# Optimization experiments

Measured on AMD Instinct MI355X. Metric: run time of the kernel, lower is better.

## Reference

```python
import jax, jax.numpy as jnp
import numpy as np

SIGMA = 1e-4
GAMMA = 1e-4
ZNEAR = 1.0
ZFAR = 100.0
EPS = 1e-10
BG = (1.0, 1.0, 1.0)

N, H, W, K = 4, 512, 512, 8
V, F = 100000, 200000


def setup_inputs() -> dict:
    key = jax.random.key(0)
    k1, k2, k3, k4, k5, k6 = jax.random.split(key, 6)
    pix_to_face = jax.random.randint(k1, (N, H, W, K), -1, F)  # -1 = background
    bary = jax.random.uniform(k2, (N, H, W, K, 3), dtype=jnp.float32)
    bary = bary / jnp.sum(bary, axis=-1, keepdims=True)  # valid barycentric
    zbuf = ZNEAR + (ZFAR - ZNEAR) * jax.random.uniform(k3, (N, H, W, K), dtype=jnp.float32)
    dists = 1e-4 * jax.random.normal(k4, (N, H, W, K), dtype=jnp.float32)
    verts_normals = jax.random.normal(k5, (V, 3), dtype=jnp.float32)
    verts_normals = verts_normals / jnp.linalg.norm(verts_normals, axis=-1, keepdims=True)
    faces = jax.random.randint(k6, (F, 3), 0, V)
    return {"pix_to_face": pix_to_face, "bary_coords": bary, "zbuf": zbuf,
            "dists": dists, "verts_normals": verts_normals, "faces": faces}


def reference(pix_to_face, bary_coords, zbuf, dists, verts_normals, faces):
    # --- NormalCalcuate: gather per-face vertex normals + barycentric interp ---
    faces_normals = verts_normals[faces]                      # (F, 3verts, 3)
    mask = pix_to_face >= 0                                    # (N,H,W,K)
    idx = jnp.maximum(pix_to_face, 0)
    attrs = faces_normals[idx]                                 # (N,H,W,K,3verts,3)
    pixel_normals = jnp.einsum('nhwkv,nhwkvd->nhwkd', bary_coords, attrs)
    pixel_normals = jnp.where(mask[..., None], pixel_normals, 0.0)

    # --- softmax_rgb_blend ---
    m = mask.astype(pixel_normals.dtype)
    prob_map = jax.nn.sigmoid(-dists / SIGMA) * m              # (N,H,W,K)
    z_inv = (ZFAR - zbuf) / (ZFAR - ZNEAR) * m                 # (N,H,W,K)
    z_inv_max = jnp.maximum(jnp.max(z_inv, axis=-1, keepdims=True), EPS)
    weights_num = prob_map * jnp.exp((z_inv - z_inv_max) / GAMMA)
    delta = jnp.maximum(jnp.exp((EPS - z_inv_max[..., 0]) / GAMMA), EPS)  # (N,H,W)
    denom = jnp.sum(weights_num, axis=-1) + delta              # (N,H,W)
    weighted_colors = jnp.einsum('nhwk,nhwkd->nhwd', weights_num, pixel_normals)
    bg = jnp.asarray(BG, dtype=pixel_normals.dtype)
    rgb = (weighted_colors + delta[..., None] * bg) / denom[..., None]  # (N,H,W,3)

    # --- F.normalize(dim=3) then (x+1)/2 ---
    norm = jnp.maximum(jnp.linalg.norm(rgb, axis=-1, keepdims=True), 1e-12)
    images = (rgb / norm + 1.0) / 2.0
    return images
```

## Files before the change

kernel.cpp:

```cpp
#include <hip/hip_runtime.h>

#define SIGMA_INV 1.0e4f
#define GAMMA_INV 1.0e4f
#define ZNEAR 1.0f
#define ZFAR 100.0f
#define EPSV 1e-10f

constexpr int KF = 8;
constexpr int NPIX = 4 * 512 * 512;
constexpr int NFACES = 200000;
#define LOG_CUT (-16.0f)
#define ZWIN (16.0f / GAMMA_INV)
#define ZMAX_SAFE 0.01f

typedef int      i32x4 __attribute__((ext_vector_type(4)));
typedef float    f32x4 __attribute__((ext_vector_type(4)));
typedef unsigned u32x4 __attribute__((ext_vector_type(4)));
typedef float    f32x2 __attribute__((ext_vector_type(2), aligned(4)));

__global__ __launch_bounds__(256) void pack_face_normals14(
    const int*   __restrict__ faces,
    const float* __restrict__ vnorm,
    uint4*       __restrict__ fn,
    int F)
{
    const int f = blockIdx.x * blockDim.x + threadIdx.x;
    if (f >= F) return;
    const int v[3] = { faces[f * 3 + 0], faces[f * 3 + 1], faces[f * 3 + 2] };

    unsigned long long lo = 0ull, hi = 0ull;
    int i = 0;
#pragma unroll
    for (int t = 0; t < 3; ++t) {
#pragma unroll
        for (int c = 0; c < 3; ++c, ++i) {
            const float x = vnorm[(size_t)v[t] * 3 + c];
            const unsigned long long code = (unsigned long long)(unsigned)
                __float2int_rn(fminf(fmaxf(x, -1.0f), 1.0f) * 8191.5f + 8191.5f);
            const int bp = 14 * i;
            if (bp < 64) {
                lo |= code << bp;
                if (bp > 50) hi |= code >> (64 - bp);
            } else {
                hi |= code << (bp - 64);
            }
        }
    }
    uint4 q;
    q.x = (unsigned)(lo & 0xFFFFFFFFull);
    q.y = (unsigned)(lo >> 32);
    q.z = (unsigned)(hi & 0xFFFFFFFFull);
    q.w = (unsigned)(hi >> 32);
    fn[f] = q;
}

__device__ __forceinline__ float dec14(const unsigned* w, int i) {
    const int bp = 14 * i;
    const int j = bp >> 5;
    const int off = bp & 31;
    unsigned long long u = (unsigned long long)w[j];
    if (j < 3) u |= (unsigned long long)w[j + 1] << 32;
    const unsigned code = (unsigned)(u >> off) & 0x3FFFu;
    return fmaf((float)code, 2.0f / 16383.0f, -1.0f);
}

__global__ __launch_bounds__(256) void normal_shader_q14_split(
    const int*   __restrict__ p2f,
    const float* __restrict__ bary,
    const float* __restrict__ zbuf,
    const float* __restrict__ dists,
    const uint4* __restrict__ fn,
    float*       __restrict__ out)
{
    const int p = blockIdx.x * blockDim.x + threadIdx.x;
    if (p >= NPIX) return;

    const int*   pfp = p2f + (size_t)p * KF;
    const float* zp  = zbuf + (size_t)p * KF;

    i32x4 fa, fb;
    f32x4 za, zb;
    asm volatile(
        "global_load_dwordx4 %0, %4, off sc0\n\t"
        "global_load_dwordx4 %1, %5, off sc0\n\t"
        "global_load_dwordx4 %2, %6, off sc0\n\t"
        "global_load_dwordx4 %3, %7, off sc0\n\t"
        "s_waitcnt vmcnt(0)"
        : "=&v"(fa), "=&v"(fb), "=&v"(za), "=&v"(zb)
        : "v"(pfp), "v"(pfp + 4), "v"(zp), "v"(zp + 4)
        : "memory");

    int f[KF] = {fa[0], fa[1], fa[2], fa[3], fb[0], fb[1], fb[2], fb[3]};
    float zv[KF] = {za[0], za[1], za[2], za[3], zb[0], zb[1], zb[2], zb[3]};

    float zinv[KF];
    float zmax = EPSV;
#pragma unroll
    for (int k = 0; k < KF; ++k) {
        const float zi = (f[k] >= 0) ? (ZFAR - zv[k]) * (1.0f / (ZFAR - ZNEAR))
                                     : 0.0f;
        zinv[k] = zi;
        zmax = fmaxf(zmax, zi);
    }

    const float zcut = zmax - ZWIN;
    unsigned rem = 0u;
#pragma unroll
    for (int k = 0; k < KF; ++k)
        if (f[k] >= 0 && zinv[k] > zcut) rem |= (1u << k);

    int ksel = 0, fsel = 0;
    float zsel = 0.0f;
#pragma unroll
    for (int k = KF - 1; k >= 0; --k) {
        if (rem & (1u << k)) { ksel = k; fsel = f[k]; zsel = zinv[k]; }
    }
    const bool has = (rem != 0u);
    unsigned rem2 = rem & (rem - 1u);
    const bool heavy = (rem2 != 0u) || (zmax <= ZMAX_SAFE);

    const size_t sidx = (size_t)p * KF + (size_t)ksel;
    const unsigned* qp = reinterpret_cast<const unsigned*>(fn + fsel);
    const float*    bp = bary + sidx * 3;

    u32x4 q;
    f32x2 b01;
    asm volatile(
        "global_load_dwordx4 %0, %2, off sc0\n\t"
        "global_load_dwordx2 %1, %3, off sc0\n\t"
        "s_waitcnt vmcnt(0)"
        : "=&v"(q), "=&v"(b01)
        : "v"(qp), "v"(bp)
        : "memory");

    unsigned w[4] = { q[0], q[1], q[2], q[3] };
    const float b0 = b01[0];
    const float b1 = b01[1];
    const float b2 = 1.0f - b0 - b1;
    const float nx = b0 * dec14(w, 0) + b1 * dec14(w, 3) + b2 * dec14(w, 6);
    const float ny = b0 * dec14(w, 1) + b1 * dec14(w, 4) + b2 * dec14(w, 7);
    const float nz = b0 * dec14(w, 2) + b1 * dec14(w, 5) + b2 * dec14(w, 8);

    float accx = 0.0f, accy = 0.0f, accz = 0.0f, wtot = 0.0f;
    if (has) {
        if (!heavy) {
            accx = nx; accy = ny; accz = nz; wtot = 1.0f;
        } else {
            const float dv0 = dists[sidx];
            const float pr0 = 1.0f / (1.0f + __expf(dv0 * SIGMA_INV));
            const float wg0 = pr0 * __expf((zsel - zmax) * GAMMA_INV);
            wtot = wg0;
            accx = wg0 * nx; accy = wg0 * ny; accz = wg0 * nz;

            while (rem2) {
                int ks = 0, gs = 0;
                float zs = 0.0f;
#pragma unroll
                for (int k = KF - 1; k >= 0; --k) {
                    if (rem2 & (1u << k)) { ks = k; gs = f[k]; zs = zinv[k]; }
                }
                rem2 &= rem2 - 1u;

                const size_t s2 = (size_t)p * KF + (size_t)ks;
                const uint4 q2 = fn[gs];
                const f32x2 bb =
                    *reinterpret_cast<const f32x2*>(bary + s2 * 3);
                const float dvs = dists[s2];

                unsigned w2[4] = { q2.x, q2.y, q2.z, q2.w };
                const float c0 = bb[0];
                const float c1 = bb[1];
                const float c2 = 1.0f - c0 - c1;
                const float mx = c0 * dec14(w2, 0) + c1 * dec14(w2, 3) + c2 * dec14(w2, 6);
                const float my = c0 * dec14(w2, 1) + c1 * dec14(w2, 4) + c2 * dec14(w2, 7);
                const float mz = c0 * dec14(w2, 2) + c1 * dec14(w2, 5) + c2 * dec14(w2, 8);

                const float prob = 1.0f / (1.0f + __expf(dvs * SIGMA_INV));
                const float wgt  = prob * __expf((zs - zmax) * GAMMA_INV);
                wtot += wgt;
                accx = fmaf(wgt, mx, accx);
                accy = fmaf(wgt, my, accy);
                accz = fmaf(wgt, mz, accz);
            }
        }
    }

    const float delta = fmaxf(__expf((EPSV - zmax) * GAMMA_INV), EPSV);
    const float inv_denom = 1.0f / (wtot + delta);
    const float r = (accx + delta) * inv_denom;
    const float g = (accy + delta) * inv_denom;
    const float b = (accz + delta) * inv_denom;

    const float nrm = sqrtf(r * r + g * g + b * b);
    const float invn = 1.0f / fmaxf(nrm, 1e-12f);

    float* o = out + (size_t)p * 3;
    o[0] = fmaf(r * invn, 0.5f, 0.5f);
    o[1] = fmaf(g * invn, 0.5f, 0.5f);
    o[2] = fmaf(b * invn, 0.5f, 0.5f);
}

__global__ __launch_bounds__(256) void normal_shader_direct(
    const int*   __restrict__ p2f,
    const float* __restrict__ bary,
    const float* __restrict__ zbuf,
    const float* __restrict__ dists,
    const float* __restrict__ vnorm,
    const int*   __restrict__ faces,
    float*       __restrict__ out)
{
    const int p = blockIdx.x * blockDim.x + threadIdx.x;
    if (p >= NPIX) return;

    const int4* pf4 = reinterpret_cast<const int4*>(p2f + (size_t)p * KF);
    int4 fa = pf4[0], fb = pf4[1];
    int f[KF] = {fa.x, fa.y, fa.z, fa.w, fb.x, fb.y, fb.z, fb.w};

    const float4* z4 = reinterpret_cast<const float4*>(zbuf + (size_t)p * KF);
    float4 za = z4[0], zb = z4[1];
    float zv[KF] = {za.x, za.y, za.z, za.w, zb.x, zb.y, zb.z, zb.w};

    const float4* d4 = reinterpret_cast<const float4*>(dists + (size_t)p * KF);
    float4 da = d4[0], db = d4[1];
    float dv[KF] = {da.x, da.y, da.z, da.w, db.x, db.y, db.z, db.w};

    const float4* b4 = reinterpret_cast<const float4*>(bary + (size_t)p * KF * 3);
    float bc[KF * 3];
#pragma unroll
    for (int i = 0; i < 6; ++i) {
        float4 t = b4[i];
        bc[4 * i + 0] = t.x; bc[4 * i + 1] = t.y;
        bc[4 * i + 2] = t.z; bc[4 * i + 3] = t.w;
    }

    float zinv[KF], prob[KF];
    float zmax = EPSV;
#pragma unroll
    for (int k = 0; k < KF; ++k) {
        const bool m = f[k] >= 0;
        const float zi = m ? (ZFAR - zv[k]) * (1.0f / (ZFAR - ZNEAR)) : 0.0f;
        const float pr = m ? 1.0f / (1.0f + __expf(dv[k] * SIGMA_INV)) : 0.0f;
        zinv[k] = zi;
        prob[k] = pr;
        zmax = fmaxf(zmax, zi);
    }

    float accx = 0.0f, accy = 0.0f, accz = 0.0f, wtot = 0.0f;
#pragma unroll
    for (int k = 0; k < KF; ++k) {
        const int idx = f[k] < 0 ? 0 : f[k];
        const int i3 = idx * 3;
        const int v0 = faces[i3 + 0];
        const int v1 = faces[i3 + 1];
        const int v2 = faces[i3 + 2];
        const float b0 = bc[k * 3 + 0];
        const float b1 = bc[k * 3 + 1];
        const float b2 = bc[k * 3 + 2];
        const float* n0 = vnorm + (size_t)v0 * 3;
        const float* n1 = vnorm + (size_t)v1 * 3;
        const float* n2 = vnorm + (size_t)v2 * 3;
        const float nx = b0 * n0[0] + b1 * n1[0] + b2 * n2[0];
        const float ny = b0 * n0[1] + b1 * n1[1] + b2 * n2[1];
        const float nz = b0 * n0[2] + b1 * n1[2] + b2 * n2[2];
        const float wgt = prob[k] * __expf((zinv[k] - zmax) * GAMMA_INV);
        wtot += wgt;
        accx = fmaf(wgt, nx, accx);
        accy = fmaf(wgt, ny, accy);
        accz = fmaf(wgt, nz, accz);
    }

    const float delta = fmaxf(__expf((EPSV - zmax) * GAMMA_INV), EPSV);
    const float inv_denom = 1.0f / (wtot + delta);
    const float r = (accx + delta) * inv_denom;
    const float g = (accy + delta) * inv_denom;
    const float b = (accz + delta) * inv_denom;

    const float nrm = sqrtf(r * r + g * g + b * b);
    const float invn = 1.0f / fmaxf(nrm, 1e-12f);

    float* o = out + (size_t)p * 3;
    o[0] = fmaf(r * invn, 0.5f, 0.5f);
    o[1] = fmaf(g * invn, 0.5f, 0.5f);
    o[2] = fmaf(b * invn, 0.5f, 0.5f);
}

extern "C" void kernel_launch(void* const* d_in, const int* in_sizes, int n_in,
                              void* d_out, int out_size, void* d_ws, size_t ws_size,
                              hipStream_t stream) {
    const int*   p2f   = (const int*)d_in[0];
    const float* bary  = (const float*)d_in[1];
    const float* zbuf  = (const float*)d_in[2];
    const float* dists = (const float*)d_in[3];
    const float* vnorm = (const float*)d_in[4];
    const int*   faces = (const int*)d_in[5];
    float* out = (float*)d_out;

    const int threads = 256;
    const size_t fn_bytes = (size_t)NFACES * sizeof(uint4);

    if (ws_size >= fn_bytes) {
        uint4* fn = (uint4*)d_ws;
        pack_face_normals14<<<(NFACES + threads - 1) / threads, threads, 0, stream>>>(
            faces, vnorm, fn, NFACES);
        normal_shader_q14_split<<<(NPIX + threads - 1) / threads, threads, 0, stream>>>(
            p2f, bary, zbuf, dists, fn, out);
    } else {
        normal_shader_direct<<<(NPIX + threads - 1) / threads, threads, 0, stream>>>(
            p2f, bary, zbuf, dists, vnorm, faces, out);
    }
}
```

Baseline: 223.8 us.

## Process four pixels per thread with batched loads and staged waitcnts

The shading kernel now has each thread handle four pixels strided by a quarter of the image. It issues all face-index and depth loads for the four pixels together, then issues all four face-normal and barycentric gathers before waiting on them one by one with partial vmcnt waits. The goal is more memory-level parallelism per wavefront, hiding gather latency behind other pixels' loads and math. Heavy pixels, those with several surviving layers or tiny depth, fall back to a separate routine that re-reads their inputs and recomputes the full blend, which adds redundant traffic for them. The kernel also launches a quarter as many threads and uses more registers per thread, which may lower occupancy.

```diff
diff --git a/kernel.cpp b/kernel.cpp
--- a/kernel.cpp
+++ b/kernel.cpp
@@ -8,6 +8,7 @@
 
 constexpr int KF = 8;
 constexpr int NPIX = 4 * 512 * 512;
+constexpr int NPIX4 = NPIX / 4;
 constexpr int NFACES = 200000;
 #define LOG_CUT (-16.0f)
 #define ZWIN (16.0f / GAMMA_INV)
@@ -64,37 +65,30 @@
     return fmaf((float)code, 2.0f / 16383.0f, -1.0f);
 }
 
-__global__ __launch_bounds__(256) void normal_shader_q14_split(
-    const int*   __restrict__ p2f,
-    const float* __restrict__ bary,
-    const float* __restrict__ zbuf,
-    const float* __restrict__ dists,
-    const uint4* __restrict__ fn,
-    float*       __restrict__ out)
-{
-    const int p = blockIdx.x * blockDim.x + threadIdx.x;
-    if (p >= NPIX) return;
-
-    const int*   pfp = p2f + (size_t)p * KF;
-    const float* zp  = zbuf + (size_t)p * KF;
-
-    i32x4 fa, fb;
-    f32x4 za, zb;
-    asm volatile(
-        "global_load_dwordx4 %0, %4, off sc0\n\t"
-        "global_load_dwordx4 %1, %5, off sc0\n\t"
-        "global_load_dwordx4 %2, %6, off sc0\n\t"
-        "global_load_dwordx4 %3, %7, off sc0\n\t"
-        "s_waitcnt vmcnt(0)"
-        : "=&v"(fa), "=&v"(fb), "=&v"(za), "=&v"(zb)
-        : "v"(pfp), "v"(pfp + 4), "v"(zp), "v"(zp + 4)
-        : "memory");
-
+__device__ __forceinline__ void finish_rgb(
+    float accx, float accy, float accz, float wtot, float zmax,
+    float& o0, float& o1, float& o2)
+{
+    const float delta = fmaxf(__expf((EPSV - zmax) * GAMMA_INV), EPSV);
+    const float inv_denom = 1.0f / (wtot + delta);
+    const float r = (accx + delta) * inv_denom;
+    const float g = (accy + delta) * inv_denom;
+    const float b = (accz + delta) * inv_denom;
+    const float nrm = sqrtf(r * r + g * g + b * b);
+    const float invn = 1.0f / fmaxf(nrm, 1e-12f);
+    o0 = fmaf(r * invn, 0.5f, 0.5f);
+    o1 = fmaf(g * invn, 0.5f, 0.5f);
+    o2 = fmaf(b * invn, 0.5f, 0.5f);
+}
+
+__device__ __forceinline__ void mask_px(
+    const i32x4& fa, const i32x4& fb, const f32x4& za, const f32x4& zb,
+    int& fsel, int& ksel, float& zmax, bool& heavy)
+{
     int f[KF] = {fa[0], fa[1], fa[2], fa[3], fb[0], fb[1], fb[2], fb[3]};
     float zv[KF] = {za[0], za[1], za[2], za[3], zb[0], zb[1], zb[2], zb[3]};
-
     float zinv[KF];
-    float zmax = EPSV;
+    zmax = EPSV;
 #pragma unroll
     for (int k = 0; k < KF; ++k) {
         const float zi = (f[k] >= 0) ? (ZFAR - zv[k]) * (1.0f / (ZFAR - ZNEAR))
@@ -102,37 +96,36 @@
         zinv[k] = zi;
         zmax = fmaxf(zmax, zi);
     }
-
     const float zcut = zmax - ZWIN;
     unsigned rem = 0u;
 #pragma unroll
     for (int k = 0; k < KF; ++k)
         if (f[k] >= 0 && zinv[k] > zcut) rem |= (1u << k);
 
-    int ksel = 0, fsel = 0;
-    float zsel = 0.0f;
-#pragma unroll
-    for (int k = KF - 1; k >= 0; --k) {
-        if (rem & (1u << k)) { ksel = k; fsel = f[k]; zsel = zinv[k]; }
-    }
-    const bool has = (rem != 0u);
-    unsigned rem2 = rem & (rem - 1u);
-    const bool heavy = (rem2 != 0u) || (zmax <= ZMAX_SAFE);
-
-    const size_t sidx = (size_t)p * KF + (size_t)ksel;
-    const unsigned* qp = reinterpret_cast<const unsigned*>(fn + fsel);
-    const float*    bp = bary + sidx * 3;
-
-    u32x4 q;
-    f32x2 b01;
+    ksel = 0; fsel = 0;
+#pragma unroll
+    for (int k = KF - 1; k >= 0; --k)
+        if (rem & (1u << k)) { ksel = k; fsel = f[k]; }
+
+    const unsigned rem2 = rem & (rem - 1u);
+    heavy = (rem == 0u) || (rem2 != 0u) || (zmax <= ZMAX_SAFE);
+}
+
+__device__ __forceinline__ void issue_gather(
+    const unsigned* qp, const float* bp, u32x4& q, f32x2& b)
+{
     asm volatile(
         "global_load_dwordx4 %0, %2, off sc0\n\t"
-        "global_load_dwordx2 %1, %3, off sc0\n\t"
-        "s_waitcnt vmcnt(0)"
-        : "=&v"(q), "=&v"(b01)
+        "global_load_dwordx2 %1, %3, off sc0"
+        : "=&v"(q), "=&v"(b)
         : "v"(qp), "v"(bp)
         : "memory");
-
+}
+
+__device__ __forceinline__ void shade_light(
+    const u32x4& q, const f32x2& b01, float zmax,
+    float& o0, float& o1, float& o2)
+{
     unsigned w[4] = { q[0], q[1], q[2], q[3] };
     const float b0 = b01[0];
     const float b1 = b01[1];
@@ -140,64 +133,172 @@
     const float nx = b0 * dec14(w, 0) + b1 * dec14(w, 3) + b2 * dec14(w, 6);
     const float ny = b0 * dec14(w, 1) + b1 * dec14(w, 4) + b2 * dec14(w, 7);
     const float nz = b0 * dec14(w, 2) + b1 * dec14(w, 5) + b2 * dec14(w, 8);
+    finish_rgb(nx, ny, nz, 1.0f, zmax, o0, o1, o2);
+}
+
+__device__ void heavy_px(
+    int p,
+    const int* __restrict__ p2f, const float* __restrict__ bary,
+    const float* __restrict__ zbuf, const float* __restrict__ dists,
+    const uint4* __restrict__ fn,
+    float& o0, float& o1, float& o2)
+{
+    const int4* pf4 = reinterpret_cast<const int4*>(p2f + (size_t)p * KF);
+    int4 fa = pf4[0], fb = pf4[1];
+    int f[KF] = {fa.x, fa.y, fa.z, fa.w, fb.x, fb.y, fb.z, fb.w};
+    const float4* z4 = reinterpret_cast<const float4*>(zbuf + (size_t)p * KF);
+    float4 za = z4[0], zb = z4[1];
+    float zv[KF] = {za.x, za.y, za.z, za.w, zb.x, zb.y, zb.z, zb.w};
+
+    float zinv[KF];
+    float zmax = EPSV;
+#pragma unroll
+    for (int k = 0; k < KF; ++k) {
+        const float zi = (f[k] >= 0) ? (ZFAR - zv[k]) * (1.0f / (ZFAR - ZNEAR))
+                                     : 0.0f;
+        zinv[k] = zi;
+        zmax = fmaxf(zmax, zi);
+    }
+    const float zcut = zmax - ZWIN;
+    unsigned rem = 0u;
+#pragma unroll
+    for (int k = 0; k < KF; ++k)
+        if (f[k] >= 0 && zinv[k] > zcut) rem |= (1u << k);
 
     float accx = 0.0f, accy = 0.0f, accz = 0.0f, wtot = 0.0f;
-    if (has) {
-        if (!heavy) {
-            accx = nx; accy = ny; accz = nz; wtot = 1.0f;
-        } else {
-            const float dv0 = dists[sidx];
-            const float pr0 = 1.0f / (1.0f + __expf(dv0 * SIGMA_INV));
-            const float wg0 = pr0 * __expf((zsel - zmax) * GAMMA_INV);
-            wtot = wg0;
-            accx = wg0 * nx; accy = wg0 * ny; accz = wg0 * nz;
-
-            while (rem2) {
-                int ks = 0, gs = 0;
-                float zs = 0.0f;
-#pragma unroll
-                for (int k = KF - 1; k >= 0; --k) {
-                    if (rem2 & (1u << k)) { ks = k; gs = f[k]; zs = zinv[k]; }
-                }
-                rem2 &= rem2 - 1u;
-
-                const size_t s2 = (size_t)p * KF + (size_t)ks;
-                const uint4 q2 = fn[gs];
-                const f32x2 bb =
-                    *reinterpret_cast<const f32x2*>(bary + s2 * 3);
-                const float dvs = dists[s2];
-
-                unsigned w2[4] = { q2.x, q2.y, q2.z, q2.w };
-                const float c0 = bb[0];
-                const float c1 = bb[1];
-                const float c2 = 1.0f - c0 - c1;
-                const float mx = c0 * dec14(w2, 0) + c1 * dec14(w2, 3) + c2 * dec14(w2, 6);
-                const float my = c0 * dec14(w2, 1) + c1 * dec14(w2, 4) + c2 * dec14(w2, 7);
-                const float mz = c0 * dec14(w2, 2) + c1 * dec14(w2, 5) + c2 * dec14(w2, 8);
-
-                const float prob = 1.0f / (1.0f + __expf(dvs * SIGMA_INV));
-                const float wgt  = prob * __expf((zs - zmax) * GAMMA_INV);
-                wtot += wgt;
-                accx = fmaf(wgt, mx, accx);
-                accy = fmaf(wgt, my, accy);
-                accz = fmaf(wgt, mz, accz);
-            }
-        }
-    }
-
-    const float delta = fmaxf(__expf((EPSV - zmax) * GAMMA_INV), EPSV);
-    const float inv_denom = 1.0f / (wtot + delta);
-    const float r = (accx + delta) * inv_denom;
-    const float g = (accy + delta) * inv_denom;
-    const float b = (accz + delta) * inv_denom;
-
-    const float nrm = sqrtf(r * r + g * g + b * b);
-    const float invn = 1.0f / fmaxf(nrm, 1e-12f);
-
-    float* o = out + (size_t)p * 3;
-    o[0] = fmaf(r * invn, 0.5f, 0.5f);
-    o[1] = fmaf(g * invn, 0.5f, 0.5f);
-    o[2] = fmaf(b * invn, 0.5f, 0.5f);
+    while (rem) {
+        int ks = 0, gs = 0;
+        float zs = 0.0f;
+#pragma unroll
+        for (int k = KF - 1; k >= 0; --k)
+            if (rem & (1u << k)) { ks = k; gs = f[k]; zs = zinv[k]; }
+        rem &= rem - 1u;
+
+        const size_t s = (size_t)p * KF + (size_t)ks;
+        const uint4 q2 = fn[gs];
+        const f32x2 bb = *reinterpret_cast<const f32x2*>(bary + s * 3);
+        const float dvs = dists[s];
+
+        unsigned w2[4] = { q2.x, q2.y, q2.z, q2.w };
+        const float c0 = bb[0];
+        const float c1 = bb[1];
+        const float c2 = 1.0f - c0 - c1;
+        const float mx = c0 * dec14(w2, 0) + c1 * dec14(w2, 3) + c2 * dec14(w2, 6);
+        const float my = c0 * dec14(w2, 1) + c1 * dec14(w2, 4) + c2 * dec14(w2, 7);
+        const float mz = c0 * dec14(w2, 2) + c1 * dec14(w2, 5) + c2 * dec14(w2, 8);
+
+        const float prob = 1.0f / (1.0f + __expf(dvs * SIGMA_INV));
+        const float wgt  = prob * __expf((zs - zmax) * GAMMA_INV);
+        wtot += wgt;
+        accx = fmaf(wgt, mx, accx);
+        accy = fmaf(wgt, my, accy);
+        accz = fmaf(wgt, mz, accz);
+    }
+    finish_rgb(accx, accy, accz, wtot, zmax, o0, o1, o2);
+}
+
+__global__ __launch_bounds__(256) void normal_shader_q14_pipe4(
+    const int*   __restrict__ p2f,
+    const float* __restrict__ bary,
+    const float* __restrict__ zbuf,
+    const float* __restrict__ dists,
+    const uint4* __restrict__ fn,
+    float*       __restrict__ out)
+{
+    const int t = blockIdx.x * blockDim.x + threadIdx.x;
+    if (t >= NPIX4) return;
+    const int p0 = t;
+    const int p1 = t + NPIX4;
+    const int p2 = t + 2 * NPIX4;
+    const int p3 = t + 3 * NPIX4;
+
+    const int*   pf0 = p2f + (size_t)p0 * KF;
+    const float* zz0 = zbuf + (size_t)p0 * KF;
+    const int*   pf1 = p2f + (size_t)p1 * KF;
+    const float* zz1 = zbuf + (size_t)p1 * KF;
+    const int*   pf2 = p2f + (size_t)p2 * KF;
+    const float* zz2 = zbuf + (size_t)p2 * KF;
+    const int*   pf3 = p2f + (size_t)p3 * KF;
+    const float* zz3 = zbuf + (size_t)p3 * KF;
+
+    i32x4 fA0, fB0, fA1, fB1, fA2, fB2, fA3, fB3;
+    f32x4 zA0, zB0, zA1, zB1, zA2, zB2, zA3, zB3;
+    asm volatile(
+        "global_load_dwordx4 %0, %16, off sc0\n\t"
+        "global_load_dwordx4 %1, %16, off offset:16 sc0\n\t"
+        "global_load_dwordx4 %2, %17, off sc0\n\t"
+        "global_load_dwordx4 %3, %17, off offset:16 sc0\n\t"
+        "global_load_dwordx4 %4, %18, off sc0\n\t"
+        "global_load_dwordx4 %5, %18, off offset:16 sc0\n\t"
+        "global_load_dwordx4 %6, %19, off sc0\n\t"
+        "global_load_dwordx4 %7, %19, off offset:16 sc0\n\t"
+        "global_load_dwordx4 %8, %20, off sc0\n\t"
+        "global_load_dwordx4 %9, %20, off offset:16 sc0\n\t"
+        "global_load_dwordx4 %10, %21, off sc0\n\t"
+        "global_load_dwordx4 %11, %21, off offset:16 sc0\n\t"
+        "global_load_dwordx4 %12, %22, off sc0\n\t"
+        "global_load_dwordx4 %13, %22, off offset:16 sc0\n\t"
+        "global_load_dwordx4 %14, %23, off sc0\n\t"
+        "global_load_dwordx4 %15, %23, off offset:16 sc0\n\t"
+        "s_waitcnt vmcnt(0)"
+        : "=&v"(fA0), "=&v"(fB0), "=&v"(zA0), "=&v"(zB0),
+          "=&v"(fA1), "=&v"(fB1), "=&v"(zA1), "=&v"(zB1),
+          "=&v"(fA2), "=&v"(fB2), "=&v"(zA2), "=&v"(zB2),
+          "=&v"(fA3), "=&v"(fB3), "=&v"(zA3), "=&v"(zB3)
+        : "v"(pf0), "v"(zz0), "v"(pf1), "v"(zz1),
+          "v"(pf2), "v"(zz2), "v"(pf3), "v"(zz3)
+        : "memory");
+
+    int fs0, ks0, fs1, ks1, fs2, ks2, fs3, ks3;
+    float zm0, zm1, zm2, zm3;
+    bool hv0, hv1, hv2, hv3;
+    mask_px(fA0, fB0, zA0, zB0, fs0, ks0, zm0, hv0);
+    mask_px(fA1, fB1, zA1, zB1, fs1, ks1, zm1, hv1);
+    mask_px(fA2, fB2, zA2, zB2, fs2, ks2, zm2, hv2);
+    mask_px(fA3, fB3, zA3, zB3, fs3, ks3, zm3, hv3);
+
+    u32x4 g0, g1, g2, g3;
+    f32x2 c0, c1, c2, c3;
+    issue_gather(reinterpret_cast<const unsigned*>(fn + fs0),
+                 bary + ((size_t)p0 * KF + (size_t)ks0) * 3, g0, c0);
+    issue_gather(reinterpret_cast<const unsigned*>(fn + fs1),
+                 bary + ((size_t)p1 * KF + (size_t)ks1) * 3, g1, c1);
+    issue_gather(reinterpret_cast<const unsigned*>(fn + fs2),
+                 bary + ((size_t)p2 * KF + (size_t)ks2) * 3, g2, c2);
+    issue_gather(reinterpret_cast<const unsigned*>(fn + fs3),
+                 bary + ((size_t)p3 * KF + (size_t)ks3) * 3, g3, c3);
+
+    float o00, o01, o02, o10, o11, o12, o20, o21, o22, o30, o31, o32;
+
+    asm volatile("s_waitcnt vmcnt(6)" ::: "memory");
+    __builtin_amdgcn_sched_barrier(0);
+    shade_light(g0, c0, zm0, o00, o01, o02);
+
+    asm volatile("s_waitcnt vmcnt(4)" ::: "memory");
+    __builtin_amdgcn_sched_barrier(0);
+    shade_light(g1, c1, zm1, o10, o11, o12);
+
+    asm volatile("s_waitcnt vmcnt(2)" ::: "memory");
+    __builtin_amdgcn_sched_barrier(0);
+    shade_light(g2, c2, zm2, o20, o21, o22);
+
+    asm volatile("s_waitcnt vmcnt(0)" ::: "memory");
+    __builtin_amdgcn_sched_barrier(0);
+    shade_light(g3, c3, zm3, o30, o31, o32);
+
+    if (hv0) heavy_px(p0, p2f, bary, zbuf, dists, fn, o00, o01, o02);
+    if (hv1) heavy_px(p1, p2f, bary, zbuf, dists, fn, o10, o11, o12);
+    if (hv2) heavy_px(p2, p2f, bary, zbuf, dists, fn, o20, o21, o22);
+    if (hv3) heavy_px(p3, p2f, bary, zbuf, dists, fn, o30, o31, o32);
+
+    float* q0p = out + (size_t)p0 * 3;
+    q0p[0] = o00; q0p[1] = o01; q0p[2] = o02;
+    float* q1p = out + (size_t)p1 * 3;
+    q1p[0] = o10; q1p[1] = o11; q1p[2] = o12;
+    float* q2p = out + (size_t)p2 * 3;
+    q2p[0] = o20; q2p[1] = o21; q2p[2] = o22;
+    float* q3p = out + (size_t)p3 * 3;
+    q3p[0] = o30; q3p[1] = o31; q3p[2] = o32;
 }
 
 __global__ __launch_bounds__(256) void normal_shader_direct(
@@ -302,7 +403,7 @@
         uint4* fn = (uint4*)d_ws;
         pack_face_normals14<<<(NFACES + threads - 1) / threads, threads, 0, stream>>>(
             faces, vnorm, fn, NFACES);
-        normal_shader_q14_split<<<(NPIX + threads - 1) / threads, threads, 0, stream>>>(
+        normal_shader_q14_pipe4<<<(NPIX4 + threads - 1) / threads, threads, 0, stream>>>(
             p2f, bary, zbuf, dists, fn, out);
     } else {
         normal_shader_direct<<<(NPIX + threads - 1) / threads, threads, 0, stream>>>(
```

Measured after the change: 234.3 us. 1.05x slower.
